# Optimization experiments

Hardware: AMD Instinct MI355X
Metric: run time of the kernel (lower is better)

## Reference

```python
import jax, jax.numpy as jnp
import numpy as np


def _conv3x3(x, w, b):
    # stride 1, padding 1, NCHW / OIHW
    y = jax.lax.conv_general_dilated(x, w, (1, 1), ((1, 1), (1, 1)),
                                     dimension_numbers=('NCHW', 'OIHW', 'NCHW'))
    return y + b[None, :, None, None]


def _bilinear(img, py, px):
    """Bilinear sample img [B,C,H,W] at float positions py,px [B,H,W].
    Out-of-bounds corners contribute zero (zero padding), matching DCNv2."""
    B, C, H, W = img.shape
    y0f = jnp.floor(py)
    x0f = jnp.floor(px)
    wy = (py - y0f)[:, None]  # [B,1,H,W]
    wx = (px - x0f)[:, None]
    y0 = y0f.astype(jnp.int32)
    x0 = x0f.astype(jnp.int32)
    flat = img.reshape(B, C, H * W)

    def g(iy, ix):
        valid = ((iy >= 0) & (iy < H) & (ix >= 0) & (ix < W))
        lin = (jnp.clip(iy, 0, H - 1) * W + jnp.clip(ix, 0, W - 1)).reshape(B, 1, -1)
        idx = jnp.broadcast_to(lin, (B, C, lin.shape[-1]))
        v = jnp.take_along_axis(flat, idx, axis=2).reshape(B, C, *iy.shape[1:])
        return v * valid[:, None].astype(img.dtype)

    v00 = g(y0, x0)
    v01 = g(y0, x0 + 1)
    v10 = g(y0 + 1, x0)
    v11 = g(y0 + 1, x0 + 1)
    return (v00 * (1 - wy) * (1 - wx) + v01 * (1 - wy) * wx
            + v10 * wy * (1 - wx) + v11 * wy * wx)


def _dcn(x, ow, ob, w, b):
    """Modulated deformable conv (DCNv2), 3x3, stride 1, pad 1, dg=1."""
    B, C, H, W = x.shape
    om = _conv3x3(x, ow, ob)                       # [B,27,H,W]
    o1, o2, m = jnp.split(om, 3, axis=1)
    off = jnp.concatenate([o1, o2], axis=1)        # [B,18,H,W]
    mask = jax.nn.sigmoid(m)                       # [B,9,H,W]
    oy = off[:, 0::2]                              # [B,9,H,W] y-offset per tap
    ox = off[:, 1::2]                              # [B,9,H,W] x-offset per tap
    ys = jnp.arange(H, dtype=x.dtype)[None, :, None]
    xs = jnp.arange(W, dtype=x.dtype)[None, None, :]
    acc = jnp.zeros((B, w.shape[0], H, W), x.dtype)
    for k in range(9):  # fixed small kernel-tap loop
        ky, kx = divmod(k, 3)
        py = ys + (ky - 1) + oy[:, k]
        px = xs + (kx - 1) + ox[:, k]
        v = _bilinear(x, py, px) * mask[:, k][:, None]   # [B,C,H,W]
        acc = acc + jnp.einsum('bchw,oc->bohw', v, w[:, :, ky, kx])
    return acc + b[None, :, None, None]


def setup_inputs() -> dict:
    key = jax.random.key(0)
    ks = jax.random.split(key, 8)
    B, H, W = 4, 96, 96
    x = jax.random.normal(ks[0], (B, 64, H, W), jnp.float32)

    def offw(k, cin):
        return jax.random.normal(k, (27, cin, 3, 3), jnp.float32) * 0.01

    def mainw(k, cout, cin):
        return jax.random.normal(k, (cout, cin, 3, 3), jnp.float32) * (1.0 / np.sqrt(cin * 9))

    return {
        'x': x,
        'ow1': offw(ks[1], 64), 'ob1': jnp.zeros((27,), jnp.float32),
        'w1': mainw(ks[2], 64, 64), 'b1': jnp.zeros((64,), jnp.float32),
        'ow2': offw(ks[3], 64), 'ob2': jnp.zeros((27,), jnp.float32),
        'w2': mainw(ks[4], 512, 64), 'b2': jnp.zeros((512,), jnp.float32),
        'ow3': offw(ks[5], 512), 'ob3': jnp.zeros((27,), jnp.float32),
        'w3': mainw(ks[6], 256, 512), 'b3': jnp.zeros((256,), jnp.float32),
    }


def reference(x, ow1, ob1, w1, b1, ow2, ob2, w2, b2, ow3, ob3, w3, b3):
    y = _dcn(x, ow1, ob1, w1, b1)
    y = _dcn(y, ow2, ob2, w2, b2)
    y = _dcn(y, ow3, ob3, w3, b3)
    return y
```

## Files before the change

### kernel.cpp

```cpp
#include <hip/hip_runtime.h>
#include <stdint.h>


#define HH 96
#define WW 96
#define BBATCH 4
#define HWP (HH*WW)
#define PTOT (BBATCH*HWP)

typedef _Float16 f16x8 __attribute__((ext_vector_type(8)));
typedef _Float16 h2    __attribute__((ext_vector_type(2)));
typedef float f32x4 __attribute__((ext_vector_type(4)));

union U16x8 { uint4 q; _Float16 h[8]; h2 v[4]; };
union UB    { uint4 q; f16x8 f; };
union UH4   { uint2 d; _Float16 h[4]; };

__global__ void k_nchw2nhwc(const float* __restrict__ in, _Float16* __restrict__ out){
  __shared__ float t[32][33];
  int b = blockIdx.z;
  int p0 = blockIdx.x*32, c0 = blockIdx.y*32;
  int tx = threadIdx.x, ty = threadIdx.y;
  #pragma unroll
  for(int i=0;i<32;i+=8)
    t[ty+i][tx] = in[((size_t)(b*64 + c0+ty+i))*HWP + p0+tx];
  __syncthreads();
  #pragma unroll
  for(int i=0;i<32;i+=8)
    out[((size_t)(b*HWP + p0+ty+i))*64 + c0+tx] = (_Float16)t[tx][ty+i];
}

template<int CIN>
__global__ void k_tow(const float* __restrict__ ow, _Float16* __restrict__ owT){
  int i = blockIdx.x*256 + threadIdx.x;
  if(i >= 9*32*CIN) return;
  int c = i % CIN; int j = (i/CIN)&31; int k = i/(CIN*32);
  owT[i] = (j<27) ? (_Float16)ow[((size_t)(j*CIN + c))*9 + k] : (_Float16)0.f;
}

template<int CIN,int COUT>
__global__ void k_tw(const float* __restrict__ w, _Float16* __restrict__ wTf){
  int i = blockIdx.x*256 + threadIdx.x;
  if(i >= 9*COUT*CIN) return;
  int c = i % CIN; int o = (i/CIN)%COUT; int k = i/(CIN*COUT);
  int g = c>>5, quad = (c>>3)&3, j = c&7;
  int ob = o>>4, l15 = o&15;
  size_t dst = ((((size_t)k*(CIN/32) + g)*(COUT/16) + ob)*64 + quad*16 + l15)*8 + j;
  wTf[dst] = (_Float16)w[((size_t)(o*CIN + c))*9 + k];
}

template<int CIN,int NT>
__launch_bounds__(256,2)
__global__ void k_goffs(const _Float16* __restrict__ xin, const _Float16* __restrict__ owT,
                        float* __restrict__ om){
  __shared__ __align__(16) _Float16 As[64*40];
  __shared__ __align__(16) _Float16 Bs[32*40];
  int pos0 = blockIdx.x*64;
  int K0 = blockIdx.y*NT;
  float* omo = om + (size_t)blockIdx.y*PTOT*32;
  int t = threadIdx.x;
  int lane = t&63, wave = t>>6;
  int quad = lane>>4, l15 = lane&15;
  f32x4 acc[2] = {};
  int pa = t>>2, ca = (t&3)*8;
  int P = pos0 + pa;
  int b = P/HWP, rem = P%HWP;
  int y = rem/WW, x = rem%WW;
  #pragma unroll 1
  for(int k=K0;k<K0+NT;k++){
    int iy = y + k/3 - 1, ix = x + k%3 - 1;
    bool valid = (iy>=0)&&(iy<HH)&&(ix>=0)&&(ix<WW);
    const _Float16* src = xin + (((size_t)b*HWP + iy*WW + ix)*CIN) + ca;
    #pragma unroll 1
    for(int c0=0;c0<CIN;c0+=32){
      uint4 av = make_uint4(0,0,0,0);
      if(valid) av = *(const uint4*)(src + c0);
      *(uint4*)&As[pa*40 + ca] = av;
      if(t < 128){
        int j = t>>2;
        *(uint4*)&Bs[j*40 + ca] = *(const uint4*)(owT + ((size_t)k*32 + j)*CIN + c0 + ca);
      }
      __syncthreads();
      UB afu; afu.q = *(const uint4*)&As[(wave*16 + l15)*40 + quad*8];
      #pragma unroll
      for(int ni=0;ni<2;ni++){
        UB bu; bu.q = *(const uint4*)&Bs[(ni*16 + l15)*40 + quad*8];
        acc[ni] = __builtin_amdgcn_mfma_f32_16x16x32_f16(afu.f, bu.f, acc[ni], 0,0,0);
      }
      __syncthreads();
    }
  }
  #pragma unroll
  for(int ni=0;ni<2;ni++)
    #pragma unroll
    for(int r=0;r<4;r++){
      int row = wave*16 + quad*4 + r;
      omo[(size_t)(pos0+row)*32 + ni*16 + l15] = acc[ni][r];
    }
}

template<int NS>
__global__ void k_prep(const float* __restrict__ om, const float* __restrict__ ob,
                       float* __restrict__ pym){
  int i = blockIdx.x*256 + threadIdx.x;
  if(i >= PTOT*9) return;
  int k = i%9, p = i/9;
  int rem = p%HWP;
  int y = rem/WW, x = rem%WW;
  float oy=0.f, ox=0.f, mm=0.f;
  #pragma unroll
  for(int s=0;s<NS;s++){
    const float* o = om + (size_t)s*PTOT*32 + (size_t)p*32;
    oy += o[2*k]; ox += o[2*k+1]; mm += o[18+k];
  }
  oy += ob[2*k]; ox += ob[2*k+1]; mm += ob[18+k];
  float m = 1.f/(1.f + expf(-mm));
  pym[(size_t)i*3+0] = (float)(y + k/3 - 1) + oy;
  pym[(size_t)i*3+1] = (float)(x + k%3 - 1) + ox;
  pym[(size_t)i*3+2] = m;
}

template<int CIN,int COUT,int BN,int MODE>
__launch_bounds__(256,2)
__global__ void k_gmain(const _Float16* __restrict__ xin, const float* __restrict__ pym,
                        const _Float16* __restrict__ wTf, const float* __restrict__ bias,
                        void* __restrict__ outv){
  constexpr int NW = BN/4;
  constexpr int NF = NW/16;
  constexpr int KG = CIN/32;
  constexpr int OB = COUT/16;
  constexpr int SPT = CIN/64;
  constexpr int NZ = (MODE==1) ? 3 : 1;
  constexpr int KN = (MODE==1) ? 3 : 9;
  constexpr int S = KN*SPT;
  __shared__ __align__(16) _Float16 As[2][64*72];
  int bx = blockIdx.x;
  int q = bx>>3, r = bx&7;
  int z = q - (q/NZ)*NZ;
  int lin = r*((gridDim.x>>3)/NZ) + q/NZ;
  int pos0 = lin*64;
  int o0 = blockIdx.y*BN;
  int K0 = (MODE==1) ? z*3 : 0;
  int t = threadIdx.x;
  int lane = t&63, wave = t>>6;
  int quad = lane>>4, l15 = lane&15;
  f32x4 acc[4][NF] = {};
  int pa = t>>2, ca = (t&3)*16;
  int P = pos0 + pa;
  int b = P/HWP;
  const _Float16* base = xin + (size_t)b*HWP*CIN + ca;
  const uint4* wf = (const uint4*)wTf;
  int obBase = (o0>>4) + wave*NF;

  auto tapParams = [&](int k, h2* W, int* oc){
    const float* pp = pym + ((size_t)P*9 + k)*3;
    float py = pp[0], px = pp[1], mk = pp[2];
    float y0f = floorf(py), x0f = floorf(px);
    float wy = py - y0f, wx = px - x0f;
    int iy0 = (int)y0f, ix0 = (int)x0f;
    int iy1 = iy0+1, ix1 = ix0+1;
    bool vy0 = (iy0>=0)&&(iy0<HH), vy1 = (iy1>=0)&&(iy1<HH);
    bool vx0 = (ix0>=0)&&(ix0<WW), vx1 = (ix1>=0)&&(ix1<WW);
    float w00 = (vy0&&vx0) ? (1.f-wy)*(1.f-wx)*mk : 0.f;
    float w01 = (vy0&&vx1) ? (1.f-wy)*wx*mk      : 0.f;
    float w10 = (vy1&&vx0) ? wy*(1.f-wx)*mk      : 0.f;
    float w11 = (vy1&&vx1) ? wy*wx*mk            : 0.f;
    int cy0 = min(max(iy0,0),HH-1), cy1 = min(max(iy1,0),HH-1);
    int cx0 = min(max(ix0,0),WW-1), cx1 = min(max(ix1,0),WW-1);
    W[0] = h2{(_Float16)w00,(_Float16)w00};
    W[1] = h2{(_Float16)w01,(_Float16)w01};
    W[2] = h2{(_Float16)w10,(_Float16)w10};
    W[3] = h2{(_Float16)w11,(_Float16)w11};
    oc[0] = (cy0*WW+cx0)*CIN;
    oc[1] = (cy0*WW+cx1)*CIN;
    oc[2] = (cy1*WW+cx0)*CIN;
    oc[3] = (cy1*WW+cx1)*CIN;
  };

  uint4 Bq[2][NF];
  const uint4* wB = wf + (size_t)(K0*KG)*OB*64 + lane;
  int buf = 0;

  if constexpr (SPT > 1){
    h2 Wcur[4], Wnxt[4];
    int ocCur[4], ocNxt[4];
    tapParams(K0, Wcur, ocCur);
    U16x8 ncA[4][2], ncB[4][2];
    {
      U16x8 c0v[4][2];
      #pragma unroll
      for(int c=0;c<4;c++){
        const _Float16* pp = base + ocCur[c];
        c0v[c][0].q = *(const uint4*)(pp);
        c0v[c][1].q = *(const uint4*)(pp + 8);
      }
      #pragma unroll
      for(int ks=0;ks<2;ks++)
        #pragma unroll
        for(int ni=0;ni<NF;ni++)
          Bq[ks][ni] = wB[(size_t)ks*OB*64 + (size_t)(obBase+ni)*64];
      wB += 2*OB*64;
      U16x8 rr0, rr1;
      #pragma unroll
      for(int j=0;j<4;j++){
        rr0.v[j] = c0v[0][0].v[j]*Wcur[0] + c0v[1][0].v[j]*Wcur[1] + c0v[2][0].v[j]*Wcur[2] + c0v[3][0].v[j]*Wcur[3];
        rr1.v[j] = c0v[0][1].v[j]*Wcur[0] + c0v[1][1].v[j]*Wcur[1] + c0v[2][1].v[j]*Wcur[2] + c0v[3][1].v[j]*Wcur[3];
      }
      *(uint4*)&As[0][pa*72 + ca]     = rr0.q;
      *(uint4*)&As[0][pa*72 + ca + 8] = rr1.q;
      #pragma unroll
      for(int c=0;c<4;c++){
        const _Float16* pp = base + ocCur[c] + 64;
        ncA[c][0].q = *(const uint4*)(pp);
        ncA[c][1].q = *(const uint4*)(pp + 8);
      }
    }

    auto stage = [&](int s, U16x8 (&ncC)[4][2], U16x8 (&ncN)[4][2]){
      __syncthreads();
      bool more  = (s+1 < S);
      bool more2 = (s+2 < S);
      if(s > 0 && (s % SPT) == 0){
        #pragma unroll
        for(int j=0;j<4;j++){ Wcur[j]=Wnxt[j]; ocCur[j]=ocNxt[j]; }
      }
      if(more2){
        int sm2 = (s+2) % SPT;
        if(sm2 == 0) tapParams(K0 + (s+2)/SPT, Wnxt, ocNxt);
        bool useNxt = (sm2 < 2);
        int ocS[4];
        #pragma unroll
        for(int c=0;c<4;c++) ocS[c] = useNxt ? ocNxt[c] : ocCur[c];
        int c0 = sm2*64;
        #pragma unroll
        for(int c=0;c<4;c++){
          const _Float16* pp = base + ocS[c] + c0;
          ncN[c][0].q = *(const uint4*)(pp);
          ncN[c][1].q = *(const uint4*)(pp + 8);
        }
      }
      UB afu[2][4];
      #pragma unroll
      for(int ks=0;ks<2;ks++)
        #pragma unroll
        for(int mi=0;mi<4;mi++)
          afu[ks][mi].q = *(const uint4*)&As[buf][(mi*16 + l15)*72 + ks*32 + quad*8];
      #pragma unroll
      for(int ks=0;ks<2;ks++)
        #pragma unroll
        for(int ni=0;ni<NF;ni++){
          UB bu; bu.q = Bq[ks][ni];
          #pragma unroll
          for(int mi=0;mi<4;mi++)
            acc[mi][ni] = __builtin_amdgcn_mfma_f32_16x16x32_f16(afu[ks][mi].f, bu.f, acc[mi][ni], 0,0,0);
        }
      if(more){
        #pragma unroll
        for(int ks=0;ks<2;ks++)
          #pragma unroll
          for(int ni=0;ni<NF;ni++)
            Bq[ks][ni] = wB[(size_t)ks*OB*64 + (size_t)(obBase+ni)*64];
        wB += 2*OB*64;
        bool lerpNxt = (((s+1) % SPT) == 0);
        h2 Wl[4];
        #pragma unroll
        for(int j=0;j<4;j++) Wl[j] = lerpNxt ? Wnxt[j] : Wcur[j];
        U16x8 rr0, rr1;
        #pragma unroll
        for(int j=0;j<4;j++){
          rr0.v[j] = ncC[0][0].v[j]*Wl[0] + ncC[1][0].v[j]*Wl[1] + ncC[2][0].v[j]*Wl[2] + ncC[3][0].v[j]*Wl[3];
          rr1.v[j] = ncC[0][1].v[j]*Wl[0] + ncC[1][1].v[j]*Wl[1] + ncC[2][1].v[j]*Wl[2] + ncC[3][1].v[j]*Wl[3];
        }
        *(uint4*)&As[buf^1][pa*72 + ca]     = rr0.q;
        *(uint4*)&As[buf^1][pa*72 + ca + 8] = rr1.q;
      }
      buf ^= 1;
    };

    #pragma unroll 1
    for(int ss=0; ss<S; ss+=2){
      stage(ss,   ncA, ncB);
      stage(ss+1, ncB, ncA);
    }
  } else {
    h2 Wc[4]; int oc_[4];
    h2 Wn[4]; int ocn[4];
    tapParams(K0, Wc, oc_);
    {
      U16x8 nc[4][2];
      #pragma unroll
      for(int c=0;c<4;c++){
        const _Float16* pp = base + oc_[c];
        nc[c][0].q = *(const uint4*)(pp);
        nc[c][1].q = *(const uint4*)(pp + 8);
      }
      #pragma unroll
      for(int ks=0;ks<2;ks++)
        #pragma unroll
        for(int ni=0;ni<NF;ni++)
          Bq[ks][ni] = wB[(size_t)ks*OB*64 + (size_t)(obBase+ni)*64];
      wB += 2*OB*64;
      U16x8 rr0, rr1;
      #pragma unroll
      for(int j=0;j<4;j++){
        rr0.v[j] = nc[0][0].v[j]*Wc[0] + nc[1][0].v[j]*Wc[1] + nc[2][0].v[j]*Wc[2] + nc[3][0].v[j]*Wc[3];
        rr1.v[j] = nc[0][1].v[j]*Wc[0] + nc[1][1].v[j]*Wc[1] + nc[2][1].v[j]*Wc[2] + nc[3][1].v[j]*Wc[3];
      }
      *(uint4*)&As[0][pa*72 + ca]     = rr0.q;
      *(uint4*)&As[0][pa*72 + ca + 8] = rr1.q;
    }
    if(S>1) tapParams(K0+1, Wn, ocn);

    #pragma unroll 1
    for(int s=0;s<S;s++){
      __syncthreads();
      U16x8 nc[4][2];
      bool more = (s+1 < S);
      if(more){
        #pragma unroll
        for(int c=0;c<4;c++){ Wc[c]=Wn[c]; oc_[c]=ocn[c]; }
        #pragma unroll
        for(int c=0;c<4;c++){
          const _Float16* pp = base + oc_[c];
          nc[c][0].q = *(const uint4*)(pp);
          nc[c][1].q = *(const uint4*)(pp + 8);
        }
      }
      UB afu[2][4];
      #pragma unroll
      for(int ks=0;ks<2;ks++)
        #pragma unroll
        for(int mi=0;mi<4;mi++)
          afu[ks][mi].q = *(const uint4*)&As[buf][(mi*16 + l15)*72 + ks*32 + quad*8];
      #pragma unroll
      for(int ks=0;ks<2;ks++)
        #pragma unroll
        for(int ni=0;ni<NF;ni++){
          UB bu; bu.q = Bq[ks][ni];
          #pragma unroll
          for(int mi=0;mi<4;mi++)
            acc[mi][ni] = __builtin_amdgcn_mfma_f32_16x16x32_f16(afu[ks][mi].f, bu.f, acc[mi][ni], 0,0,0);
        }
      if(more){
        #pragma unroll
        for(int ks=0;ks<2;ks++)
          #pragma unroll
          for(int ni=0;ni<NF;ni++)
            Bq[ks][ni] = wB[(size_t)ks*OB*64 + (size_t)(obBase+ni)*64];
        wB += 2*OB*64;
        if(s+2 < S) tapParams(K0+s+2, Wn, ocn);
        U16x8 rr0, rr1;
        #pragma unroll
        for(int j=0;j<4;j++){
          rr0.v[j] = nc[0][0].v[j]*Wc[0] + nc[1][0].v[j]*Wc[1] + nc[2][0].v[j]*Wc[2] + nc[3][0].v[j]*Wc[3];
          rr1.v[j] = nc[0][1].v[j]*Wc[0] + nc[1][1].v[j]*Wc[1] + nc[2][1].v[j]*Wc[2] + nc[3][1].v[j]*Wc[3];
        }
        *(uint4*)&As[buf^1][pa*72 + ca]     = rr0.q;
        *(uint4*)&As[buf^1][pa*72 + ca + 8] = rr1.q;
      }
      buf ^= 1;
    }
  }

  #pragma unroll
  for(int mi=0;mi<4;mi++){
    #pragma unroll
    for(int ni=0;ni<NF;ni++){
      int col = o0 + wave*NW + ni*16 + l15;
      if(MODE==1){
        float* out = (float*)outv + (size_t)z*PTOT*COUT;
        #pragma unroll
        for(int r=0;r<4;r++){
          int row = pos0 + mi*16 + quad*4 + r;
          out[(size_t)row*COUT + col] = acc[mi][ni][r];
        }
      } else {
        float bo = bias[col];
        _Float16* out = (_Float16*)outv;
        #pragma unroll
        for(int r=0;r<4;r++){
          int row = pos0 + mi*16 + quad*4 + r;
          out[(size_t)row*COUT + col] = (_Float16)(acc[mi][ni][r]+bo);
        }
      }
    }
  }
}

template<int COUT>
__global__ void k_redA(const float* __restrict__ part, const float* __restrict__ bias,
                       _Float16* __restrict__ out){
  int i4 = blockIdx.x*256 + threadIdx.x;
  constexpr int N4 = PTOT*COUT/4;
  if(i4 >= N4) return;
  const float4* p = (const float4*)part;
  float4 a = p[i4], b = p[i4 + N4], c = p[i4 + 2*N4];
  int col0 = (i4*4) & (COUT-1);
  float4 bi = *(const float4*)(bias + col0);
  UH4 r;
  r.h[0] = (_Float16)(a.x+b.x+c.x+bi.x);
  r.h[1] = (_Float16)(a.y+b.y+c.y+bi.y);
  r.h[2] = (_Float16)(a.z+b.z+c.z+bi.z);
  r.h[3] = (_Float16)(a.w+b.w+c.w+bi.w);
  *(uint2*)(out + (size_t)i4*4) = r.d;
}

__global__ void k_redT(const float* __restrict__ part, const float* __restrict__ bias,
                       float* __restrict__ out){
  __shared__ float t[32][33];
  constexpr int COUT = 256;
  constexpr size_t SL = (size_t)PTOT*COUT;
  int b = blockIdx.z;
  int p0 = blockIdx.x*32, c0 = blockIdx.y*32;
  int tx = threadIdx.x, ty = threadIdx.y;
  #pragma unroll
  for(int i=0;i<32;i+=8){
    size_t idx = ((size_t)(b*HWP + p0+ty+i))*COUT + c0+tx;
    t[ty+i][tx] = part[idx] + part[idx+SL] + part[idx+2*SL];
  }
  __syncthreads();
  #pragma unroll
  for(int i=0;i<32;i+=8)
    out[((size_t)(b*COUT + c0+ty+i))*HWP + p0+tx] = t[tx][ty+i] + bias[c0+ty+i];
}

extern "C" void kernel_launch(void* const* d_in, const int* in_sizes, int n_in,
                              void* d_out, int out_size, void* d_ws, size_t ws_size,
                              hipStream_t stream){
  (void)in_sizes; (void)n_in; (void)out_size;
  const float* x   = (const float*)d_in[0];
  const float* ow1 = (const float*)d_in[1];
  const float* ob1 = (const float*)d_in[2];
  const float* w1  = (const float*)d_in[3];
  const float* b1  = (const float*)d_in[4];
  const float* ow2 = (const float*)d_in[5];
  const float* ob2 = (const float*)d_in[6];
  const float* w2  = (const float*)d_in[7];
  const float* b2  = (const float*)d_in[8];
  const float* ow3 = (const float*)d_in[9];
  const float* ob3 = (const float*)d_in[10];
  const float* w3  = (const float*)d_in[11];
  const float* b3  = (const float*)d_in[12];

  char* p = (char*)d_ws;
  auto carve = [&](size_t bytes)->char*{ char* r = p; p += (bytes + 255) & ~(size_t)255; return r; };
  _Float16* xh  = (_Float16*)carve((size_t)PTOT*64*2);
  _Float16* y1  = (_Float16*)carve((size_t)PTOT*64*2);
  _Float16* y2  = (_Float16*)carve((size_t)PTOT*512*2);
  _Float16* owT = (_Float16*)carve((size_t)9*32*512*2);
  _Float16* wT  = (_Float16*)carve((size_t)9*512*512*2);
  float*    om  = (float*)carve((size_t)3*PTOT*32*4);
  float*    pym = (float*)carve((size_t)PTOT*9*3*4);
  bool splitK = ws_size >= ((size_t)p - (size_t)d_ws) + (size_t)3*PTOT*256*4 + 4096;
  float* part = splitK ? (float*)carve((size_t)3*PTOT*256*4) : nullptr;

  k_nchw2nhwc<<<dim3(288,2,BBATCH), dim3(32,8), 0, stream>>>(x, xh);

  if(splitK){
    k_tow<64><<<(9*32*64+255)/256,256,0,stream>>>(ow1, owT);
    k_tw<64,64><<<(9*64*64+255)/256,256,0,stream>>>(w1, wT);
    k_goffs<64,3><<<dim3(PTOT/64,3),256,0,stream>>>(xh, owT, om);
    k_prep<3><<<(PTOT*9+255)/256,256,0,stream>>>(om, ob1, pym);
    k_gmain<64,64,64,1><<<dim3(3*PTOT/64,1,1),256,0,stream>>>(xh, pym, wT, b1, part);
    k_redA<64><<<(PTOT*64/4+255)/256,256,0,stream>>>(part, b1, y1);

    k_tow<64><<<(9*32*64+255)/256,256,0,stream>>>(ow2, owT);
    k_tw<64,512><<<(9*512*64+255)/256,256,0,stream>>>(w2, wT);
    k_goffs<64,3><<<dim3(PTOT/64,3),256,0,stream>>>(y1, owT, om);
    k_prep<3><<<(PTOT*9+255)/256,256,0,stream>>>(om, ob2, pym);
    k_gmain<64,512,256,0><<<dim3(PTOT/64,2),256,0,stream>>>(y1, pym, wT, b2, y2);

    k_tow<512><<<(9*32*512+255)/256,256,0,stream>>>(ow3, owT);
    k_tw<512,256><<<(9*256*512+255)/256,256,0,stream>>>(w3, wT);
    k_goffs<512,3><<<dim3(PTOT/64,3),256,0,stream>>>(y2, owT, om);
    k_prep<3><<<(PTOT*9+255)/256,256,0,stream>>>(om, ob3, pym);
    k_gmain<512,256,256,1><<<dim3(3*PTOT/64,1,1),256,0,stream>>>(y2, pym, wT, b3, part);
    k_redT<<<dim3(288,8,4),dim3(32,8),0,stream>>>(part, b3, (float*)d_out);
  } else {
    k_tow<64><<<(9*32*64+255)/256,256,0,stream>>>(ow1, owT);
    k_tw<64,64><<<(9*64*64+255)/256,256,0,stream>>>(w1, wT);
    k_goffs<64,9><<<dim3(PTOT/64,1),256,0,stream>>>(xh, owT, om);
    k_prep<1><<<(PTOT*9+255)/256,256,0,stream>>>(om, ob1, pym);
    k_gmain<64,64,64,0><<<dim3(PTOT/64,1),256,0,stream>>>(xh, pym, wT, b1, y1);

    k_tow<64><<<(9*32*64+255)/256,256,0,stream>>>(ow2, owT);
    k_tw<64,512><<<(9*512*64+255)/256,256,0,stream>>>(w2, wT);
    k_goffs<64,9><<<dim3(PTOT/64,1),256,0,stream>>>(y1, owT, om);
    k_prep<1><<<(PTOT*9+255)/256,256,0,stream>>>(om, ob2, pym);
    k_gmain<64,512,256,0><<<dim3(PTOT/64,2),256,0,stream>>>(y1, pym, wT, b2, y2);

    k_tow<512><<<(9*32*512+255)/256,256,0,stream>>>(ow3, owT);
    k_tw<512,256><<<(9*256*512+255)/256,256,0,stream>>>(w3, wT);
    k_goffs<512,9><<<dim3(PTOT/64,1),256,0,stream>>>(y2, owT, om);
    k_prep<1><<<(PTOT*9+255)/256,256,0,stream>>>(om, ob3, pym);
    k_gmain<512,256,256,0><<<dim3(PTOT/64,1),256,0,stream>>>(y2, pym, wT, b3, y1);
    {
      struct L { static __global__ void tr(const _Float16* in, float* out){
        int i = blockIdx.x*256 + threadIdx.x;
        if(i >= PTOT*256) return;
        int c = i & 255, pnt = i >> 8;
        int bb = pnt / HWP, pr = pnt % HWP;
        out[((size_t)bb*256 + c)*HWP + pr] = (float)in[i];
      }};
      hipLaunchKernelGGL(L::tr, dim3((PTOT*256+255)/256), dim3(256), 0, stream,
                         (const _Float16*)y1, (float*)d_out);
    }
  }
}
```

Baseline: 400.3 us.

## Double-buffer and register-prefetch offset conv GEMM for wide-input layers

For input channel counts of 128 or more (the 512-channel third DCN layer), the offset/mask conv kernel now loads 64-channel K-chunks into double-buffered shared memory. It prefetches global loads two stages ahead in registers, so each iteration needs only one barrier instead of two. The aim is to hide global memory latency and cut synchronization overhead in this small-N GEMM. The cost is more LDS and register use, which may lower occupancy, and more complex indexing. Smaller-CIN layers keep the original path.

Measured after the change: 590.6 us. 47.5% more time.

```diff
diff --git a/kernel.cpp b/kernel.cpp
--- a/kernel.cpp
+++ b/kernel.cpp
@@ -53,8 +53,6 @@
 __launch_bounds__(256,2)
 __global__ void k_goffs(const _Float16* __restrict__ xin, const _Float16* __restrict__ owT,
                         float* __restrict__ om){
-  __shared__ __align__(16) _Float16 As[64*40];
-  __shared__ __align__(16) _Float16 Bs[32*40];
   int pos0 = blockIdx.x*64;
   int K0 = blockIdx.y*NT;
   float* omo = om + (size_t)blockIdx.y*PTOT*32;
@@ -62,34 +60,111 @@
   int lane = t&63, wave = t>>6;
   int quad = lane>>4, l15 = lane&15;
   f32x4 acc[2] = {};
-  int pa = t>>2, ca = (t&3)*8;
-  int P = pos0 + pa;
-  int b = P/HWP, rem = P%HWP;
-  int y = rem/WW, x = rem%WW;
-  #pragma unroll 1
-  for(int k=K0;k<K0+NT;k++){
-    int iy = y + k/3 - 1, ix = x + k%3 - 1;
-    bool valid = (iy>=0)&&(iy<HH)&&(ix>=0)&&(ix<WW);
-    const _Float16* src = xin + (((size_t)b*HWP + iy*WW + ix)*CIN) + ca;
+
+  if constexpr (CIN >= 128){
+    constexpr int SPT = CIN/64;
+    constexpr int S = NT*SPT;
+    __shared__ __align__(16) _Float16 As[2][64*72];
+    __shared__ __align__(16) _Float16 Bs[2][32*72];
+    int pa = t>>2, ca = (t&3)*16;
+    int jb = t>>3, cb = (t&7)*8;
+    int P = pos0 + pa;
+    int b = P/HWP, rem = P%HWP;
+    int y = rem/WW, x = rem%WW;
+    const _Float16* srcC; bool vldC; int ktC;
+    const _Float16* srcN; bool vldN; int ktN;
+    auto tapSet = [&](int k, const _Float16*& src, bool& vld, int& kt){
+      int iy = y + k/3 - 1, ix = x + k%3 - 1;
+      vld = (iy>=0)&&(iy<HH)&&(ix>=0)&&(ix<WW);
+      int cy = min(max(iy,0),HH-1), cx = min(max(ix,0),WW-1);
+      src = xin + ((size_t)b*HWP + cy*WW + cx)*CIN + ca;
+      kt = k;
+    };
+    struct Regs { uint4 a0,a1,bv; };
+    Regs rA, rB;
+    auto loadSet = [&](Regs& R, const _Float16* src, bool vld, int kt, int c0){
+      uint4 z = make_uint4(0,0,0,0);
+      uint4 x0 = *(const uint4*)(src + c0);
+      uint4 x1 = *(const uint4*)(src + c0 + 8);
+      R.a0 = vld ? x0 : z;
+      R.a1 = vld ? x1 : z;
+      R.bv = *(const uint4*)(owT + ((size_t)kt*32 + jb)*CIN + c0 + cb);
+    };
+    auto writeSet = [&](const Regs& R, int dbuf){
+      *(uint4*)&As[dbuf][pa*72 + ca]     = R.a0;
+      *(uint4*)&As[dbuf][pa*72 + ca + 8] = R.a1;
+      *(uint4*)&Bs[dbuf][jb*72 + cb]     = R.bv;
+    };
+
+    tapSet(K0, srcC, vldC, ktC);
+    { Regs r0; loadSet(r0, srcC, vldC, ktC, 0); writeSet(r0, 0); }
+    loadSet(rA, srcC, vldC, ktC, 64);
+    int buf = 0;
+
+    auto stage = [&](int s, Regs& C, Regs& N){
+      __syncthreads();
+      if(s > 0 && (s % SPT) == 0){ srcC = srcN; vldC = vldN; ktC = ktN; }
+      if(s+2 < S){
+        int sm2 = (s+2) % SPT;
+        if(sm2 == 0) tapSet(K0 + (s+2)/SPT, srcN, vldN, ktN);
+        bool useN = (sm2 < 2);
+        const _Float16* src = useN ? srcN : srcC;
+        bool vld = useN ? vldN : vldC;
+        int kt  = useN ? ktN  : ktC;
+        loadSet(N, src, vld, kt, sm2*64);
+      }
+      UB afu0, afu1;
+      afu0.q = *(const uint4*)&As[buf][(wave*16 + l15)*72 + quad*8];
+      afu1.q = *(const uint4*)&As[buf][(wave*16 + l15)*72 + 32 + quad*8];
+      #pragma unroll
+      for(int ni=0;ni<2;ni++){
+        UB bu0, bu1;
+        bu0.q = *(const uint4*)&Bs[buf][(ni*16 + l15)*72 + quad*8];
+        bu1.q = *(const uint4*)&Bs[buf][(ni*16 + l15)*72 + 32 + quad*8];
+        acc[ni] = __builtin_amdgcn_mfma_f32_16x16x32_f16(afu0.f, bu0.f, acc[ni], 0,0,0);
+        acc[ni] = __builtin_amdgcn_mfma_f32_16x16x32_f16(afu1.f, bu1.f, acc[ni], 0,0,0);
+      }
+      if(s+1 < S) writeSet(C, buf^1);
+      buf ^= 1;
+    };
     #pragma unroll 1
-    for(int c0=0;c0<CIN;c0+=32){
-      uint4 av = make_uint4(0,0,0,0);
-      if(valid) av = *(const uint4*)(src + c0);
-      *(uint4*)&As[pa*40 + ca] = av;
-      if(t < 128){
-        int j = t>>2;
-        *(uint4*)&Bs[j*40 + ca] = *(const uint4*)(owT + ((size_t)k*32 + j)*CIN + c0 + ca);
-      }
-      __syncthreads();
-      UB afu; afu.q = *(const uint4*)&As[(wave*16 + l15)*40 + quad*8];
-      #pragma unroll
-      for(int ni=0;ni<2;ni++){
-        UB bu; bu.q = *(const uint4*)&Bs[(ni*16 + l15)*40 + quad*8];
-        acc[ni] = __builtin_amdgcn_mfma_f32_16x16x32_f16(afu.f, bu.f, acc[ni], 0,0,0);
-      }
-      __syncthreads();
+    for(int ss=0; ss<S; ss+=2){
+      stage(ss,   rA, rB);
+      stage(ss+1, rB, rA);
+    }
+  } else {
+    __shared__ __align__(16) _Float16 As[64*40];
+    __shared__ __align__(16) _Float16 Bs[32*40];
+    int pa = t>>2, ca = (t&3)*8;
+    int P = pos0 + pa;
+    int b = P/HWP, rem = P%HWP;
+    int y = rem/WW, x = rem%WW;
+    #pragma unroll 1
+    for(int k=K0;k<K0+NT;k++){
+      int iy = y + k/3 - 1, ix = x + k%3 - 1;
+      bool valid = (iy>=0)&&(iy<HH)&&(ix>=0)&&(ix<WW);
+      const _Float16* src = xin + (((size_t)b*HWP + iy*WW + ix)*CIN) + ca;
+      #pragma unroll 1
+      for(int c0=0;c0<CIN;c0+=32){
+        uint4 av = make_uint4(0,0,0,0);
+        if(valid) av = *(const uint4*)(src + c0);
+        *(uint4*)&As[pa*40 + ca] = av;
+        if(t < 128){
+          int j = t>>2;
+          *(uint4*)&Bs[j*40 + ca] = *(const uint4*)(owT + ((size_t)k*32 + j)*CIN + c0 + ca);
+        }
+        __syncthreads();
+        UB afu; afu.q = *(const uint4*)&As[(wave*16 + l15)*40 + quad*8];
+        #pragma unroll
+        for(int ni=0;ni<2;ni++){
+          UB bu; bu.q = *(const uint4*)&Bs[(ni*16 + l15)*40 + quad*8];
+          acc[ni] = __builtin_amdgcn_mfma_f32_16x16x32_f16(afu.f, bu.f, acc[ni], 0,0,0);
+        }
+        __syncthreads();
+      }
     }
   }
+
   #pragma unroll
   for(int ni=0;ni<2;ni++)
     #pragma unroll
```
